# Optimization experiments

Measured on AMD Instinct MI355X. Metric: run time of the kernel, lower is better.

The kernel has to match this reference:

```python
import jax, jax.numpy as jnp
import numpy as np
from jax import lax

B, L, LQ, D_IN, ET, H, INIT_EMBED = 16, 256, 64, 32, 128, 4, 8
DIM = 2 * D_IN          # attention value/feature dim (x concat mask)
ETK = ET // H           # per-head time-embedding dim


def _lin(key, fan_in, shape):
    b = 1.0 / np.sqrt(fan_in)
    return jax.random.uniform(key, shape, jnp.float32, -b, b)


def setup_inputs() -> dict:
    key = jax.random.key(0)
    ks = jax.random.split(key, 24)
    inp = {
        "x": jax.random.normal(ks[0], (B, L, D_IN), jnp.float32),
        "time_steps": jnp.sort(jax.random.uniform(ks[1], (B, L), jnp.float32), axis=-1),
        "mask": (jax.random.uniform(ks[2], (B, L, D_IN)) > 0.5).astype(jnp.float32),
        "query": jnp.linspace(0.0, 1.0, LQ, dtype=jnp.float32),
        # time embedding: Linear(1,1) and Linear(1, ET-1)
        "w_lin": _lin(ks[3], 1, (1,)), "b_lin": _lin(ks[4], 1, (1,)),
        "w_per": _lin(ks[5], 1, (ET - 1,)), "b_per": _lin(ks[6], 1, (ET - 1,)),
        # attention projections (stored as (in,out))
        "Wq": _lin(ks[7], ET, (ET, ET)), "bq": _lin(ks[8], ET, (ET,)),
        "Wk": _lin(ks[9], ET, (ET, ET)), "bk": _lin(ks[10], ET, (ET,)),
        "Wo": _lin(ks[11], H * DIM, (H * DIM, ET)), "bo": _lin(ks[12], H * DIM, (ET,)),
        # vanilla RNN (tanh)
        "W_ih": _lin(ks[13], ET, (ET, ET)), "b_ih": _lin(ks[14], ET, (ET,)),
        "W_hh": _lin(ks[15], ET, (ET, ET)), "b_hh": _lin(ks[16], ET, (ET,)),
        "r1_w": _lin(ks[17], ET, (ET, 128)), "r1_b": _lin(ks[17], ET, (128,)),
        "r2_w": _lin(ks[18], 128, (128, 128)), "r2_b": _lin(ks[18], 128, (128,)),
        "r3_w": _lin(ks[19], 128, (128, ET)), "r3_b": _lin(ks[19], 128, (ET,)),
        "r4_w": _lin(ks[20], ET, (ET, INIT_EMBED)), "r4_b": _lin(ks[20], ET, (INIT_EMBED,)),
    }
    return inp


def reference(x, time_steps, mask, query,
              w_lin, b_lin, w_per, b_per,
              Wq, bq, Wk, bk, Wo, bo,
              W_ih, b_ih, W_hh, b_hh,
              r1_w, r1_b, r2_w, r2_b, r3_w, r3_b, r4_w, r4_b):
    def time_embed(tt):  # (...,) -> (..., ET)
        tt = tt[..., None]
        return jnp.concatenate([tt * w_lin + b_lin,
                                jnp.sin(tt * w_per + b_per)], axis=-1)

    xc = jnp.concatenate([x, mask], axis=-1)          # (B,L,DIM) value
    m2 = jnp.concatenate([mask, mask], axis=-1)       # (B,L,DIM)

    kemb = time_embed(time_steps)                     # (B,L,ET)
    qemb = time_embed(query)                          # (LQ,ET)

    q = (qemb @ Wq + bq).reshape(LQ, H, ETK).transpose(1, 0, 2)       # (H,LQ,ETK)
    k = (kemb @ Wk + bk).reshape(B, L, H, ETK).transpose(0, 2, 1, 3)  # (B,H,L,ETK)

    scores = jnp.einsum('hqe,bhke->bhqk', q, k) / np.sqrt(ETK)        # (B,H,LQ,L)
    # per-feature mask broadcast: (B,H,LQ,L,DIM)
    s5 = jnp.where(m2[:, None, None, :, :] == 0, -1e9, scores[..., None])
    p = jax.nn.softmax(s5, axis=-2)                   # softmax over keys L
    att = jnp.einsum('bhqkd,bkd->bhqd', p, xc)        # (B,H,LQ,DIM)
    att = att.transpose(0, 2, 1, 3).reshape(B, LQ, H * DIM)
    out = att @ Wo + bo                               # (B,LQ,ET)

    # vanilla tanh RNN, return final hidden state
    def step(h, xt):
        h = jnp.tanh(xt @ W_ih + b_ih + h @ W_hh + b_hh)
        return h, None
    h0 = jnp.zeros((B, ET), out.dtype)
    hT, _ = lax.scan(step, h0, out.transpose(1, 0, 2))  # scan over LQ

    y = hT @ r1_w + r1_b
    y = y @ r2_w + r2_b
    y = y @ r3_w + r3_b
    y = y @ r4_w + r4_b                               # (B, INIT_EMBED)
    return y
```

## Files before the change

### kernel.cpp

```cpp
#include <hip/hip_runtime.h>
#include <hip/hip_bf16.h>


#define NB 16
#define NL 256
#define NLQ 64
#define NDIN 32
#define NET 128
#define NH 4
#define NETK 32

__global__ __launch_bounds__(128) void k_embed_proj(
    const float* __restrict__ ts, const float* __restrict__ query,
    const float* __restrict__ w_lin, const float* __restrict__ b_lin,
    const float* __restrict__ w_per, const float* __restrict__ b_per,
    const float* __restrict__ Wk, const float* __restrict__ bk,
    const float* __restrict__ Wq, const float* __restrict__ bq,
    float* __restrict__ kproj, float* __restrict__ qproj) {
  __shared__ float emb[8 * NET];
  int g = blockIdx.x;
  int j = threadIdx.x;
  bool isQ = (g >= 512);
  int base = (isQ ? g - 512 : g) * 8;
  float wl_ = w_lin[0], bl_ = b_lin[0];
  float wp = (j > 0) ? w_per[j - 1] : 0.f;
  float bp = (j > 0) ? b_per[j - 1] : 0.f;
#pragma unroll
  for (int rr = 0; rr < 8; rr++) {
    float t = isQ ? query[base + rr] : ts[base + rr];
    emb[rr * NET + j] = (j == 0) ? (t * wl_ + bl_) : sinf(t * wp + bp);
  }
  __syncthreads();
  const float* W = isQ ? Wq : Wk;
  float bias = isQ ? bq[j] : bk[j];
  float acc[8];
#pragma unroll
  for (int rr = 0; rr < 8; rr++) acc[rr] = bias;
#pragma unroll 4
  for (int i = 0; i < NET; i++) {
    float wv = W[i * NET + j];
#pragma unroll
    for (int rr = 0; rr < 8; rr++) acc[rr] += emb[rr * NET + i] * wv;
  }
  float* dst = isQ ? qproj : kproj;
#pragma unroll
  for (int rr = 0; rr < 8; rr++) dst[(size_t)(base + rr) * NET + j] = acc[rr];
}

__global__ __launch_bounds__(256) void k_attn(
    const float* __restrict__ x, const float* __restrict__ mask,
    const float* __restrict__ qproj, const float* __restrict__ kproj,
    float* __restrict__ att) {
  const float SC = 0.17677669529663687f;
  int blk = blockIdx.x;
  int qg = blk & 15;
  int h  = (blk >> 4) & 3;
  int b  = blk >> 6;
  int t  = threadIdx.x;

  __shared__ float xs[NL * NDIN];
  __shared__ unsigned mb[NL];
  __shared__ float es[4 * NL];
  __shared__ float qs[4 * NETK];

  if (t < 128) {
    int qq = t >> 5, i = t & 31;
    qs[t] = qproj[(qg * 4 + qq) * NET + h * NETK + i];
  }
  {
    const float4* src = (const float4*)(x + (size_t)b * NL * NDIN);
    float4* dst = (float4*)xs;
#pragma unroll
    for (int u = 0; u < 8; u++) dst[t + 256 * u] = src[t + 256 * u];
  }
  {
    const float4* mr4 = (const float4*)(mask + (size_t)(b * NL + t) * NDIN);
    unsigned bits = 0;
#pragma unroll
    for (int u = 0; u < 8; u++) {
      float4 m = mr4[u];
      bits |= (m.x != 0.f ? 1u : 0u) << (4 * u);
      bits |= (m.y != 0.f ? 1u : 0u) << (4 * u + 1);
      bits |= (m.z != 0.f ? 1u : 0u) << (4 * u + 2);
      bits |= (m.w != 0.f ? 1u : 0u) << (4 * u + 3);
    }
    mb[t] = bits;
  }
  __syncthreads();

  {
    float kr[NETK];
    const float4* kp =
        (const float4*)(kproj + (size_t)(b * NL + t) * NET + h * NETK);
#pragma unroll
    for (int i = 0; i < 8; i++) {
      float4 v = kp[i];
      kr[4 * i] = v.x; kr[4 * i + 1] = v.y;
      kr[4 * i + 2] = v.z; kr[4 * i + 3] = v.w;
    }
#pragma unroll
    for (int qq = 0; qq < 4; qq++) {
      const float* qv = &qs[qq * NETK];
      float s0 = 0.f, s1 = 0.f;
#pragma unroll
      for (int i = 0; i < NETK; i += 2) {
        s0 += qv[i] * kr[i];
        s1 += qv[i + 1] * kr[i + 1];
      }
      es[qq * NL + t] = __expf((s0 + s1) * SC);
    }
  }
  __syncthreads();

  {
    int s = t & 1;
    int p = t >> 1;
    int qq = p >> 5;
    int c  = p & 31;
    int k0 = s * 128;
    float den = 0.f, num = 0.f, sumx = 0.f;
#pragma unroll 4
    for (int k = k0; k < k0 + 128; k++) {
      float e  = es[qq * NL + k];
      float mv = ((mb[k] >> c) & 1u) ? 1.f : 0.f;
      float xv = xs[k * NDIN + c];
      sumx += xv;
      e *= mv;
      den += e;
      num += e * xv;
    }
    den  += __shfl_xor(den, 1, 64);
    num  += __shfl_xor(num, 1, 64);
    sumx += __shfl_xor(sumx, 1, 64);
    if (s == 0) {
      bool any = (den > 0.f);
      float ax = any ? (num / den) : (sumx * (1.f / 256.f));
      float am = any ? 1.f : 0.f;
      int q = qg * 4 + qq;
      float* ao = att + (size_t)((b * NLQ + q) * NH + h) * 64;
      ao[c]      = ax;
      ao[32 + c] = am;
    }
  }
}

__global__ __launch_bounds__(128) void k_out_xw(
    const float* __restrict__ att,
    const float* __restrict__ Wo, const float* __restrict__ bo,
    const float* __restrict__ Wih, const float* __restrict__ bih,
    const float* __restrict__ bhh, float* __restrict__ XW) {
  int r = blockIdx.x;
  int j = threadIdx.x;
  __shared__ float arow[NH * 64];
  __shared__ float orow[NET];
  arow[j]       = att[(size_t)r * 256 + j];
  arow[j + 128] = att[(size_t)r * 256 + 128 + j];
  __syncthreads();
  float a0 = bo[j], a1 = 0.f, a2 = 0.f, a3 = 0.f;
#pragma unroll 8
  for (int u = 0; u < 256; u += 4) {
    a0 += arow[u]     * Wo[(u)     * NET + j];
    a1 += arow[u + 1] * Wo[(u + 1) * NET + j];
    a2 += arow[u + 2] * Wo[(u + 2) * NET + j];
    a3 += arow[u + 3] * Wo[(u + 3) * NET + j];
  }
  orow[j] = (a0 + a1) + (a2 + a3);
  __syncthreads();
  float b0 = bih[j] + bhh[j], b1 = 0.f, b2 = 0.f, b3 = 0.f;
#pragma unroll 8
  for (int e = 0; e < NET; e += 4) {
    b0 += orow[e]     * Wih[(e)     * NET + j];
    b1 += orow[e + 1] * Wih[(e + 1) * NET + j];
    b2 += orow[e + 2] * Wih[(e + 2) * NET + j];
    b3 += orow[e + 3] * Wih[(e + 3) * NET + j];
  }
  XW[(size_t)r * NET + j] = (b0 + b1) + (b2 + b3);
}

__device__ __forceinline__ void layer128(const float* src_lds,
                                         const float* __restrict__ W,
                                         const float* __restrict__ bvec,
                                         float* dst_lds, int j, int s) {
  const float4* h4 = (const float4*)(src_lds + s * 64);
  float a0 = 0.f, a1 = 0.f, a2 = 0.f, a3 = 0.f;
#pragma unroll
  for (int i = 0; i < 16; i++) {
    float4 hv = h4[i];
    int base = (s * 64 + 4 * i) * NET + j;
    a0 += hv.x * W[base];
    a1 += hv.y * W[base + NET];
    a2 += hv.z * W[base + 2 * NET];
    a3 += hv.w * W[base + 3 * NET];
  }
  float acc = (a0 + a1) + (a2 + a3);
  acc += __shfl_xor(acc, 1, 64);
  if (s == 0) dst_lds[j] = acc + bvec[j];
}

__global__ __launch_bounds__(256, 1) void k_rnn(
    const float* __restrict__ XW, const float* __restrict__ Whh,
    const float* __restrict__ r1w, const float* __restrict__ r1b,
    const float* __restrict__ r2w, const float* __restrict__ r2b,
    const float* __restrict__ r3w, const float* __restrict__ r3b,
    const float* __restrict__ r4w, const float* __restrict__ r4b,
    float* __restrict__ out) {
  int b = blockIdx.x;
  int tid = threadIdx.x;
  int s = tid & 1;
  int j = tid >> 1;
  __shared__ float hb[2][NET];
  __shared__ float tmp[NET];

  float w[64];
#pragma unroll
  for (int i = 0; i < 64; i++) w[i] = Whh[(s * 64 + i) * NET + j];
  float xw[32];
#pragma unroll
  for (int u = 0; u < 32; u++)
    xw[u] = XW[(size_t)(b * NLQ + 2 * u + s) * NET + j];

  hb[0][tid & 127] = 0.f;
  __syncthreads();

#pragma unroll 2
  for (int t = 0; t < NLQ; t++) {
    const float4* h4 = (const float4*)&hb[t & 1][s * 64];
    float a0 = 0.f, a1 = 0.f, a2 = 0.f, a3 = 0.f;
#pragma unroll
    for (int i = 0; i < 16; i++) {
      float4 hv = h4[i];
      a0 += hv.x * w[4 * i];
      a1 += hv.y * w[4 * i + 1];
      a2 += hv.z * w[4 * i + 2];
      a3 += hv.w * w[4 * i + 3];
    }
    float acc = (a0 + a1) + (a2 + a3);
    acc += __shfl_xor(acc, 1, 64);
    if (s == (t & 1)) {
      float z = acc + xw[t >> 1];
      float e2 = __expf(2.f * z);
      hb[(t + 1) & 1][j] = 1.f - 2.f / (e2 + 1.f);
    }
    __syncthreads();
  }

  layer128(hb[0], r1w, r1b, tmp, j, s);
  __syncthreads();
  layer128(tmp, r2w, r2b, hb[1], j, s);
  __syncthreads();
  layer128(hb[1], r3w, r3b, hb[0], j, s);
  __syncthreads();
  if (tid < 64) {
    int jj = tid >> 3, p = tid & 7;
    float y = 0.f;
#pragma unroll
    for (int i = 0; i < 16; i++) {
      int ii = p * 16 + i;
      y += hb[0][ii] * r4w[ii * 8 + jj];
    }
    y += __shfl_xor(y, 1, 64);
    y += __shfl_xor(y, 2, 64);
    y += __shfl_xor(y, 4, 64);
    if (p == 0) out[b * 8 + jj] = y + r4b[jj];
  }
}

extern "C" void kernel_launch(void* const* d_in, const int* in_sizes, int n_in,
                              void* d_out, int out_size, void* d_ws, size_t ws_size,
                              hipStream_t stream) {
  const float* x     = (const float*)d_in[0];
  const float* ts    = (const float*)d_in[1];
  const float* mask  = (const float*)d_in[2];
  const float* query = (const float*)d_in[3];
  const float* w_lin = (const float*)d_in[4];
  const float* b_lin = (const float*)d_in[5];
  const float* w_per = (const float*)d_in[6];
  const float* b_per = (const float*)d_in[7];
  const float* Wq    = (const float*)d_in[8];
  const float* bq    = (const float*)d_in[9];
  const float* Wk    = (const float*)d_in[10];
  const float* bk    = (const float*)d_in[11];
  const float* Wo    = (const float*)d_in[12];
  const float* bo    = (const float*)d_in[13];
  const float* Wih   = (const float*)d_in[14];
  const float* bih   = (const float*)d_in[15];
  const float* Whh   = (const float*)d_in[16];
  const float* bhh   = (const float*)d_in[17];
  const float* r1w   = (const float*)d_in[18];
  const float* r1b   = (const float*)d_in[19];
  const float* r2w   = (const float*)d_in[20];
  const float* r2b   = (const float*)d_in[21];
  const float* r3w   = (const float*)d_in[22];
  const float* r3b   = (const float*)d_in[23];
  const float* r4w   = (const float*)d_in[24];
  const float* r4b   = (const float*)d_in[25];
  float* out = (float*)d_out;

  float* ws    = (float*)d_ws;
  float* kproj = ws;
  float* qproj = ws + 524288;
  float* att   = ws + 532480;
  float* XW    = ws + 794624;

  k_embed_proj<<<520, 128, 0, stream>>>(
      ts, query, w_lin, b_lin, w_per, b_per, Wk, bk, Wq, bq, kproj, qproj);
  k_attn<<<NB * NH * 16, 256, 0, stream>>>(x, mask, qproj, kproj, att);
  k_out_xw<<<NB * NLQ, 128, 0, stream>>>(att, Wo, bo, Wih, bih, bhh, XW);
  k_rnn<<<NB, 256, 0, stream>>>(XW, Whh, r1w, r1b, r2w, r2b, r3w, r3b,
                                r4w, r4b, out);
}
```

Baseline: 187.3 us.

## Run RNN with one thread per hidden unit, XW staged in LDS

The recurrent kernel moves from 256 threads (two threads per hidden unit, joined by a shuffle) to 128 threads, each holding a full 128-entry column of W_hh in registers. The whole per-batch XW slab is staged in shared memory instead of per-thread register arrays, and the dot product uses eight accumulators. The regressor layers are rewritten as plain per-thread loops. This removes the cross-lane shuffle and halves the waves per step, but each thread does twice the serial FMAs per timestep and register pressure rises, which could cause spilling.

```diff
diff --git a/kernel.cpp b/kernel.cpp
--- a/kernel.cpp
+++ b/kernel.cpp
@@ -177,27 +177,7 @@
   XW[(size_t)r * NET + j] = (b0 + b1) + (b2 + b3);
 }
 
-__device__ __forceinline__ void layer128(const float* src_lds,
-                                         const float* __restrict__ W,
-                                         const float* __restrict__ bvec,
-                                         float* dst_lds, int j, int s) {
-  const float4* h4 = (const float4*)(src_lds + s * 64);
-  float a0 = 0.f, a1 = 0.f, a2 = 0.f, a3 = 0.f;
-#pragma unroll
-  for (int i = 0; i < 16; i++) {
-    float4 hv = h4[i];
-    int base = (s * 64 + 4 * i) * NET + j;
-    a0 += hv.x * W[base];
-    a1 += hv.y * W[base + NET];
-    a2 += hv.z * W[base + 2 * NET];
-    a3 += hv.w * W[base + 3 * NET];
-  }
-  float acc = (a0 + a1) + (a2 + a3);
-  acc += __shfl_xor(acc, 1, 64);
-  if (s == 0) dst_lds[j] = acc + bvec[j];
-}
-
-__global__ __launch_bounds__(256, 1) void k_rnn(
+__global__ __launch_bounds__(128, 1) void k_rnn(
     const float* __restrict__ XW, const float* __restrict__ Whh,
     const float* __restrict__ r1w, const float* __restrict__ r1b,
     const float* __restrict__ r2w, const float* __restrict__ r2b,
@@ -205,58 +185,95 @@
     const float* __restrict__ r4w, const float* __restrict__ r4b,
     float* __restrict__ out) {
   int b = blockIdx.x;
-  int tid = threadIdx.x;
-  int s = tid & 1;
-  int j = tid >> 1;
+  int j = threadIdx.x;
+  __shared__ float xwl[NLQ * NET];
   __shared__ float hb[2][NET];
   __shared__ float tmp[NET];
 
-  float w[64];
-#pragma unroll
-  for (int i = 0; i < 64; i++) w[i] = Whh[(s * 64 + i) * NET + j];
-  float xw[32];
-#pragma unroll
-  for (int u = 0; u < 32; u++)
-    xw[u] = XW[(size_t)(b * NLQ + 2 * u + s) * NET + j];
-
-  hb[0][tid & 127] = 0.f;
-  __syncthreads();
-
-#pragma unroll 2
+  {
+    const float4* src = (const float4*)(XW + (size_t)b * NLQ * NET);
+    float4* dst = (float4*)xwl;
+#pragma unroll
+    for (int u = 0; u < 16; u++) dst[j + 128 * u] = src[j + 128 * u];
+  }
+  float w[NET];
+#pragma unroll
+  for (int i = 0; i < NET; i++) w[i] = Whh[i * NET + j];
+
+  hb[0][j] = 0.f;
+  __syncthreads();
+
   for (int t = 0; t < NLQ; t++) {
-    const float4* h4 = (const float4*)&hb[t & 1][s * 64];
+    const float4* h4 = (const float4*)hb[t & 1];
     float a0 = 0.f, a1 = 0.f, a2 = 0.f, a3 = 0.f;
+    float a4 = 0.f, a5 = 0.f, a6 = 0.f, a7 = 0.f;
 #pragma unroll
     for (int i = 0; i < 16; i++) {
-      float4 hv = h4[i];
-      a0 += hv.x * w[4 * i];
-      a1 += hv.y * w[4 * i + 1];
-      a2 += hv.z * w[4 * i + 2];
-      a3 += hv.w * w[4 * i + 3];
-    }
-    float acc = (a0 + a1) + (a2 + a3);
-    acc += __shfl_xor(acc, 1, 64);
-    if (s == (t & 1)) {
-      float z = acc + xw[t >> 1];
-      float e2 = __expf(2.f * z);
-      hb[(t + 1) & 1][j] = 1.f - 2.f / (e2 + 1.f);
-    }
+      float4 hv = h4[2 * i];
+      float4 hw = h4[2 * i + 1];
+      a0 += hv.x * w[8 * i];
+      a1 += hv.y * w[8 * i + 1];
+      a2 += hv.z * w[8 * i + 2];
+      a3 += hv.w * w[8 * i + 3];
+      a4 += hw.x * w[8 * i + 4];
+      a5 += hw.y * w[8 * i + 5];
+      a6 += hw.z * w[8 * i + 6];
+      a7 += hw.w * w[8 * i + 7];
+    }
+    float acc = ((a0 + a1) + (a2 + a3)) + ((a4 + a5) + (a6 + a7));
+    float z = acc + xwl[t * NET + j];
+    float e2 = __expf(2.f * z);
+    hb[(t + 1) & 1][j] = 1.f - 2.f / (e2 + 1.f);
     __syncthreads();
   }
 
-  layer128(hb[0], r1w, r1b, tmp, j, s);
-  __syncthreads();
-  layer128(tmp, r2w, r2b, hb[1], j, s);
-  __syncthreads();
-  layer128(hb[1], r3w, r3b, hb[0], j, s);
-  __syncthreads();
-  if (tid < 64) {
-    int jj = tid >> 3, p = tid & 7;
+  {
+    float a0 = r1b[j], a1 = 0.f, a2 = 0.f, a3 = 0.f;
+#pragma unroll 8
+    for (int i = 0; i < NET; i += 4) {
+      a0 += hb[0][i]     * r1w[(i)     * NET + j];
+      a1 += hb[0][i + 1] * r1w[(i + 1) * NET + j];
+      a2 += hb[0][i + 2] * r1w[(i + 2) * NET + j];
+      a3 += hb[0][i + 3] * r1w[(i + 3) * NET + j];
+    }
+    tmp[j] = (a0 + a1) + (a2 + a3);
+  }
+  __syncthreads();
+  {
+    float a0 = r2b[j], a1 = 0.f, a2 = 0.f, a3 = 0.f;
+#pragma unroll 8
+    for (int i = 0; i < NET; i += 4) {
+      a0 += tmp[i]     * r2w[(i)     * NET + j];
+      a1 += tmp[i + 1] * r2w[(i + 1) * NET + j];
+      a2 += tmp[i + 2] * r2w[(i + 2) * NET + j];
+      a3 += tmp[i + 3] * r2w[(i + 3) * NET + j];
+    }
+    float v = (a0 + a1) + (a2 + a3);
+    __syncthreads();
+    hb[1][j] = v;
+  }
+  __syncthreads();
+  {
+    float a0 = r3b[j], a1 = 0.f, a2 = 0.f, a3 = 0.f;
+#pragma unroll 8
+    for (int i = 0; i < NET; i += 4) {
+      a0 += hb[1][i]     * r3w[(i)     * NET + j];
+      a1 += hb[1][i + 1] * r3w[(i + 1) * NET + j];
+      a2 += hb[1][i + 2] * r3w[(i + 2) * NET + j];
+      a3 += hb[1][i + 3] * r3w[(i + 3) * NET + j];
+    }
+    float v = (a0 + a1) + (a2 + a3);
+    __syncthreads();
+    tmp[j] = v;
+  }
+  __syncthreads();
+  if (j < 64) {
+    int jj = j >> 3, p = j & 7;
     float y = 0.f;
 #pragma unroll
     for (int i = 0; i < 16; i++) {
       int ii = p * 16 + i;
-      y += hb[0][ii] * r4w[ii * 8 + jj];
+      y += tmp[ii] * r4w[ii * 8 + jj];
     }
     y += __shfl_xor(y, 1, 64);
     y += __shfl_xor(y, 2, 64);
@@ -306,6 +323,6 @@
       ts, query, w_lin, b_lin, w_per, b_per, Wk, bk, Wq, bq, kproj, qproj);
   k_attn<<<NB * NH * 16, 256, 0, stream>>>(x, mask, qproj, kproj, att);
   k_out_xw<<<NB * NLQ, 128, 0, stream>>>(att, Wo, bo, Wih, bih, bhh, XW);
-  k_rnn<<<NB, 256, 0, stream>>>(XW, Whh, r1w, r1b, r2w, r2b, r3w, r3b,
+  k_rnn<<<NB, 128, 0, stream>>>(XW, Whh, r1w, r1b, r2w, r2b, r3w, r3b,
                                 r4w, r4b, out);
 }
```

After: 201.0 us. 7.3% more time.
